# Optimization experiments

Measured on AMD Instinct MI355X. Metric: run time of the kernel, lower is better.

The kernel has to match this reference:

```python
import jax, jax.numpy as jnp
import numpy as np

B, C, H, W = 8, 64, 112, 112
O, K, PAD, STRIDE = 64, 3, 1, 1
KK = K * K
OH = (H - K + 2 * PAD) // STRIDE + 1
OW = (W - K + 2 * PAD) // STRIDE + 1
L = OH * OW  # number of patches


def setup_inputs() -> dict:
    key = jax.random.key(0)
    k1, k2, k3 = jax.random.split(key, 3)
    x = jax.random.normal(k1, (B, C, H, W), dtype=jnp.float32)
    weight = jax.random.normal(k2, (O, C, K, K), dtype=jnp.float32)
    # one uniformly random kernel position to zero out, per patch (nums=1)
    mask_idx = jax.random.randint(k3, (L,), 0, KK, dtype=jnp.int32)
    return {"x": x, "weight": weight, "mask_idx": mask_idx}


def reference(x, weight, mask_idx):
    b = x.shape[0]
    # im2col: [b, C*KK, OH, OW], feature dim ordered channel-major (c, kh, kw)
    # which matches torch.nn.Unfold ordering.
    patches = jax.lax.conv_general_dilated_patches(
        x, (K, K), (STRIDE, STRIDE), ((PAD, PAD), (PAD, PAD)))
    patches = patches.reshape(b, C * KK, L)  # [b, CK, L]

    # Per-patch mask over kernel positions, tiled across channels
    # (equivalent to mask.repeat(1, in_channels) in the original).
    mask = jnp.ones((L, KK), dtype=x.dtype).at[jnp.arange(L), mask_idx].set(0.0)
    mask_full = jnp.tile(mask, (1, C))  # [L, C*KK]

    # weight.view(O, -1).t() -> [CK, O]; masking the weight rows per patch is
    # mathematically identical to masking the unfolded input per patch, which
    # avoids materializing the [L, CK, O] masked weight tensor.
    w2 = weight.reshape(O, C * KK).T  # [CK, O]
    out = jnp.einsum('bkl,lk,ko->bol', patches, mask_full, w2)  # [b, O, L]
    return out.reshape(b, O, OH, OW)
```

## Files before the change

kernel.cpp:

```cpp
#include <hip/hip_runtime.h>
#include <hip/hip_bf16.h>
#include <cstdint>

#define Bn 8
#define Cn 64
#define Hn 112
#define Wn 112
#define On 64
#define Ln (Hn * Wn)
#define HP 114
#define WP 114

typedef __attribute__((ext_vector_type(4)))  float f32x4;
typedef __attribute__((ext_vector_type(16))) float f32x16;
typedef __attribute__((ext_vector_type(8)))  short bf16x8;
typedef __attribute__((ext_vector_type(4)))  unsigned int u32x4;

__device__ __forceinline__ unsigned f2bf(float f) {
    unsigned u = __float_as_uint(f);
    unsigned r = 0x7fffu + ((u >> 16) & 1u);
    return (u + r) >> 16;
}

__global__ __launch_bounds__(64) void wpack_kernel(const float* __restrict__ w,
                                                   unsigned short* __restrict__ wpk) {
    int idx = blockIdx.x;
    int kc = idx & 3, wr = (idx >> 2) & 1, p = idx >> 3;
    int lane = threadIdx.x;
    int o  = wr * 32 + (lane & 31);
    int cb = kc * 16 + (lane >> 5) * 8;
    unsigned pk[4];
#pragma unroll
    for (int j = 0; j < 4; j++) {
        float v0 = w[((size_t)o * Cn + cb + 2 * j) * 9 + p];
        float v1 = w[((size_t)o * Cn + cb + 2 * j + 1) * 9 + p];
        pk[j] = f2bf(v0) | (f2bf(v1) << 16);
    }
    u32x4 v; v[0] = pk[0]; v[1] = pk[1]; v[2] = pk[2]; v[3] = pk[3];
    reinterpret_cast<u32x4*>(wpk)[idx * 64 + lane] = v;
}

__global__ __launch_bounds__(512, 4) void conv_fused(const float* __restrict__ x,
                                                     const unsigned short* __restrict__ wpk,
                                                     const int* __restrict__ mask_idx,
                                                     float* __restrict__ out) {
    __shared__ char xs[4 * WP * Cn * 2];

    int b  = blockIdx.x & 7;
    int lt = blockIdx.x >> 3;
    int l0 = lt * 128;
    int oh0 = l0 / Wn;

    int tid  = threadIdx.x;
    int wave = tid >> 6, lane = tid & 63;
    int wr = wave >> 2;
    int wc = wave & 3;
    int hi = lane >> 5;

    int lg = l0 + wc * 32 + (lane & 31);
    int oh = lg / Wn, ow = lg - oh * Wn;
    int r  = oh - oh0;
    int mv = mask_idx[lg];

    const u32x4* wv = reinterpret_cast<const u32x4*>(wpk);
    u32x4 apre[2][4];
#pragma unroll
    for (int kc = 0; kc < 4; ++kc) apre[0][kc] = wv[((0 * 2 + wr) * 4 + kc) * 64 + lane];
#pragma unroll
    for (int kc = 0; kc < 4; ++kc) apre[1][kc] = wv[((1 * 2 + wr) * 4 + kc) * 64 + lane];

    const float* xb = x + (size_t)b * Cn * Hn * Wn;
#pragma unroll
    for (int it = 0; it < 8; ++it) {
        int q = tid + it * 512;
        if (q < 4 * 8 * WP) {
            int row = q / (8 * WP);
            int rem = q - row * (8 * WP);
            int c8  = rem / WP;
            int wp  = rem - c8 * WP;
            int h = oh0 + row - 1;
            int w = wp - 1;
            bool inb = ((unsigned)h < (unsigned)Hn) & ((unsigned)w < (unsigned)Wn);
            const float* s = xb + ((size_t)(c8 * 8) * Hn + (inb ? h : 0)) * Wn + (inb ? w : 0);
            unsigned pk[4];
#pragma unroll
            for (int j = 0; j < 4; ++j) {
                float v0 = s[(size_t)(2 * j)     * (Hn * Wn)];
                float v1 = s[(size_t)(2 * j + 1) * (Hn * Wn)];
                if (!inb) { v0 = 0.f; v1 = 0.f; }
                pk[j] = f2bf(v0) | (f2bf(v1) << 16);
            }
            int qs = (row * WP + wp) * 8 + c8;
            int off = (qs * 16) ^ ((wp & 7) << 4);
            u32x4 v; v[0] = pk[0]; v[1] = pk[1]; v[2] = pk[2]; v[3] = pk[3];
            *reinterpret_cast<u32x4*>(xs + off) = v;
        }
    }

    f32x16 acc = {};
    const u32x4 vzero = {0u, 0u, 0u, 0u};

    __syncthreads();

#pragma unroll
    for (int p = 0; p < 9; ++p) {
        int dh = p / 3, dw = p - dh * 3;

        int wq   = ow + dw;
        int base = ((r + dh) * WP + wq) << 7;
        int swz  = (wq & 7) << 4;
        u32x4 bv[4];
#pragma unroll
        for (int kc = 0; kc < 4; ++kc) {
            int off = (base + ((2 * kc + hi) << 4)) ^ swz;
            bv[kc] = *reinterpret_cast<const u32x4*>(xs + off);
        }
        if (mv == p) { bv[0] = vzero; bv[1] = vzero; bv[2] = vzero; bv[3] = vzero; }

#pragma unroll
        for (int kc = 0; kc < 4; ++kc) {
            bf16x8 a = *reinterpret_cast<bf16x8*>(&apre[p & 1][kc]);
            bf16x8 bb = *reinterpret_cast<bf16x8*>(&bv[kc]);
            acc = __builtin_amdgcn_mfma_f32_32x32x16_bf16(a, bb, acc, 0, 0, 0);
        }

        if (p < 7) {
#pragma unroll
            for (int kc = 0; kc < 4; ++kc)
                apre[p & 1][kc] = wv[(((p + 2) * 2 + wr) * 4 + kc) * 64 + lane];
        }
    }

    float* ob = out + (size_t)(b * On + wr * 32) * Ln + lg;
#pragma unroll
    for (int reg = 0; reg < 16; ++reg) {
        int orow = (reg & 3) + 8 * (reg >> 2) + 4 * hi;
        ob[(size_t)orow * Ln] = acc[reg];
    }
}

extern "C" void kernel_launch(void* const* d_in, const int* in_sizes, int n_in,
                              void* d_out, int out_size, void* d_ws, size_t ws_size,
                              hipStream_t stream) {
    const float* x    = (const float*)d_in[0];
    const float* w    = (const float*)d_in[1];
    const int*   mask = (const int*)d_in[2];
    float* out = (float*)d_out;

    unsigned short* wpk = (unsigned short*)d_ws;

    wpack_kernel<<<72,      64,  0, stream>>>(w, wpk);
    conv_fused  <<<Bn * 98, 512, 0, stream>>>(x, wpk, mask, out);
}
```

Before: 95.28 us.

## Pre-pack padded bf16 input in prep kernel and stream tiles via global_load_lds

A separate prep pass now converts x into a zero-padded, channel-swizzled bf16 NHWC buffer in workspace, merged into one launch with the weight packing. The conv kernel then fills its LDS tile with direct global_load_lds copies instead of strided fp32 gathers and per-element conversion. This removes redundant halo-row conversion and strided reads from the main kernel. In exchange it adds a full write and re-read of a roughly 13 MB intermediate buffer and an extra pass over x.

```diff
diff --git a/kernel.cpp b/kernel.cpp
--- a/kernel.cpp
+++ b/kernel.cpp
@@ -16,34 +16,70 @@
 typedef __attribute__((ext_vector_type(8)))  short bf16x8;
 typedef __attribute__((ext_vector_type(4)))  unsigned int u32x4;
 
+typedef __attribute__((address_space(3))) unsigned int lds_u32;
+typedef __attribute__((address_space(1))) const unsigned int glob_u32;
+
 __device__ __forceinline__ unsigned f2bf(float f) {
     unsigned u = __float_as_uint(f);
     unsigned r = 0x7fffu + ((u >> 16) & 1u);
     return (u + r) >> 16;
 }
 
-__global__ __launch_bounds__(64) void wpack_kernel(const float* __restrict__ w,
+__global__ __launch_bounds__(128) void prep_kernel(const float* __restrict__ x,
+                                                   const float* __restrict__ w,
+                                                   unsigned short* __restrict__ xps,
                                                    unsigned short* __restrict__ wpk) {
-    int idx = blockIdx.x;
-    int kc = idx & 3, wr = (idx >> 2) & 1, p = idx >> 3;
-    int lane = threadIdx.x;
-    int o  = wr * 32 + (lane & 31);
-    int cb = kc * 16 + (lane >> 5) * 8;
-    unsigned pk[4];
+    int blk = blockIdx.x;
+    int t = threadIdx.x;
+    if (blk < 912) {
+        int b = blk / HP, row = blk - b * HP;
+        int c8  = t >> 4;
+        int wpl = t & 15;
+        int h = row - 1;
+        const float* xb = x + (size_t)b * Cn * Hn * Wn;
+        unsigned short* dst = xps + ((size_t)(b * HP + row) * WP) * Cn;
 #pragma unroll
-    for (int j = 0; j < 4; j++) {
-        float v0 = w[((size_t)o * Cn + cb + 2 * j) * 9 + p];
-        float v1 = w[((size_t)o * Cn + cb + 2 * j + 1) * 9 + p];
-        pk[j] = f2bf(v0) | (f2bf(v1) << 16);
+        for (int g = 0; g < 8; ++g) {
+            int wp = wpl + (g << 4);
+            if (wp < WP) {
+                int wcol = wp - 1;
+                bool inb = ((unsigned)h < (unsigned)Hn) & ((unsigned)wcol < (unsigned)Wn);
+                const float* s = xb + ((size_t)(c8 * 8) * Hn + (inb ? h : 0)) * Wn + (inb ? wcol : 0);
+                unsigned pk[4];
+#pragma unroll
+                for (int j = 0; j < 4; ++j) {
+                    float v0 = s[(size_t)(2 * j)     * (Hn * Wn)];
+                    float v1 = s[(size_t)(2 * j + 1) * (Hn * Wn)];
+                    if (!inb) { v0 = 0.f; v1 = 0.f; }
+                    pk[j] = f2bf(v0) | (f2bf(v1) << 16);
+                }
+                int slot = c8 ^ (wp & 7);
+                u32x4 v; v[0] = pk[0]; v[1] = pk[1]; v[2] = pk[2]; v[3] = pk[3];
+                *reinterpret_cast<u32x4*>(dst + ((size_t)wp * 8 + slot) * 8) = v;
+            }
+        }
+    } else {
+        int idx = (blk - 912) * 2 + (t >> 6);
+        int lane = t & 63;
+        int kc = idx & 3, wr2 = (idx >> 2) & 1, p = idx >> 3;
+        int o  = wr2 * 32 + (lane & 31);
+        int cb = kc * 16 + (lane >> 5) * 8;
+        unsigned pk[4];
+#pragma unroll
+        for (int j = 0; j < 4; ++j) {
+            float v0 = w[((size_t)o * Cn + cb + 2 * j) * 9 + p];
+            float v1 = w[((size_t)o * Cn + cb + 2 * j + 1) * 9 + p];
+            pk[j] = f2bf(v0) | (f2bf(v1) << 16);
+        }
+        u32x4 v; v[0] = pk[0]; v[1] = pk[1]; v[2] = pk[2]; v[3] = pk[3];
+        reinterpret_cast<u32x4*>(wpk)[idx * 64 + lane] = v;
     }
-    u32x4 v; v[0] = pk[0]; v[1] = pk[1]; v[2] = pk[2]; v[3] = pk[3];
-    reinterpret_cast<u32x4*>(wpk)[idx * 64 + lane] = v;
 }
 
-__global__ __launch_bounds__(512, 4) void conv_fused(const float* __restrict__ x,
-                                                     const unsigned short* __restrict__ wpk,
-                                                     const int* __restrict__ mask_idx,
-                                                     float* __restrict__ out) {
+__global__ __launch_bounds__(512, 4) void conv_mfma(const unsigned short* __restrict__ xps,
+                                                    const unsigned short* __restrict__ wpk,
+                                                    const int* __restrict__ mask_idx,
+                                                    float* __restrict__ out) {
     __shared__ char xs[4 * WP * Cn * 2];
 
     int b  = blockIdx.x & 7;
@@ -62,40 +98,27 @@
     int r  = oh - oh0;
     int mv = mask_idx[lg];
 
+    {
+        const char* gsrc = (const char*)(xps + ((size_t)(b * HP + oh0) * WP) * Cn);
+        int cb0 = wave * 456;
+#pragma unroll
+        for (int i = 0; i < 8; ++i) {
+            int cbase = cb0 + i * 64;
+            if (i < 7 || lane < 8) {
+                __builtin_amdgcn_global_load_lds(
+                    (glob_u32*)(gsrc + ((size_t)(cbase + lane) << 4)),
+                    reinterpret_cast<lds_u32*>(reinterpret_cast<uintptr_t>(xs + ((size_t)cbase << 4))),
+                    16, 0, 0);
+            }
+        }
+    }
+
     const u32x4* wv = reinterpret_cast<const u32x4*>(wpk);
     u32x4 apre[2][4];
 #pragma unroll
-    for (int kc = 0; kc < 4; ++kc) apre[0][kc] = wv[((0 * 2 + wr) * 4 + kc) * 64 + lane];
+    for (int kc = 0; kc < 4; ++kc) apre[0][kc] = wv[(wr * 4 + kc) * 64 + lane];
 #pragma unroll
-    for (int kc = 0; kc < 4; ++kc) apre[1][kc] = wv[((1 * 2 + wr) * 4 + kc) * 64 + lane];
-
-    const float* xb = x + (size_t)b * Cn * Hn * Wn;
-#pragma unroll
-    for (int it = 0; it < 8; ++it) {
-        int q = tid + it * 512;
-        if (q < 4 * 8 * WP) {
-            int row = q / (8 * WP);
-            int rem = q - row * (8 * WP);
-            int c8  = rem / WP;
-            int wp  = rem - c8 * WP;
-            int h = oh0 + row - 1;
-            int w = wp - 1;
-            bool inb = ((unsigned)h < (unsigned)Hn) & ((unsigned)w < (unsigned)Wn);
-            const float* s = xb + ((size_t)(c8 * 8) * Hn + (inb ? h : 0)) * Wn + (inb ? w : 0);
-            unsigned pk[4];
-#pragma unroll
-            for (int j = 0; j < 4; ++j) {
-                float v0 = s[(size_t)(2 * j)     * (Hn * Wn)];
-                float v1 = s[(size_t)(2 * j + 1) * (Hn * Wn)];
-                if (!inb) { v0 = 0.f; v1 = 0.f; }
-                pk[j] = f2bf(v0) | (f2bf(v1) << 16);
-            }
-            int qs = (row * WP + wp) * 8 + c8;
-            int off = (qs * 16) ^ ((wp & 7) << 4);
-            u32x4 v; v[0] = pk[0]; v[1] = pk[1]; v[2] = pk[2]; v[3] = pk[3];
-            *reinterpret_cast<u32x4*>(xs + off) = v;
-        }
-    }
+    for (int kc = 0; kc < 4; ++kc) apre[1][kc] = wv[((2 + wr) * 4 + kc) * 64 + lane];
 
     f32x16 acc = {};
     const u32x4 vzero = {0u, 0u, 0u, 0u};
@@ -119,7 +142,7 @@
 
 #pragma unroll
         for (int kc = 0; kc < 4; ++kc) {
-            bf16x8 a = *reinterpret_cast<bf16x8*>(&apre[p & 1][kc]);
+            bf16x8 a  = *reinterpret_cast<bf16x8*>(&apre[p & 1][kc]);
             bf16x8 bb = *reinterpret_cast<bf16x8*>(&bv[kc]);
             acc = __builtin_amdgcn_mfma_f32_32x32x16_bf16(a, bb, acc, 0, 0, 0);
         }
@@ -147,8 +170,9 @@
     const int*   mask = (const int*)d_in[2];
     float* out = (float*)d_out;
 
-    unsigned short* wpk = (unsigned short*)d_ws;
+    unsigned short* xps = (unsigned short*)d_ws;
+    unsigned short* wpk = (unsigned short*)((char*)d_ws + 13307904);
 
-    wpack_kernel<<<72,      64,  0, stream>>>(w, wpk);
-    conv_fused  <<<Bn * 98, 512, 0, stream>>>(x, wpk, mask, out);
+    prep_kernel<<<948,     128, 0, stream>>>(x, w, xps, wpk);
+    conv_mfma  <<<Bn * 98, 512, 0, stream>>>(xps, wpk, mask, out);
 }
```

Measured after the change: 97.73 us. +2.6%, slower.

## Halve block to 256 threads, each wave computing all 64 output channels

Applied to the files above, without the earlier changes.

Each block now has four waves instead of eight, and each wave covers 32 patches for both 32-channel output halves, using two accumulators. Every B fragment read from LDS therefore feeds two MFMAs, which halves LDS reads per MFMA. Weight fragments for one kernel position are prefetched a step ahead into double-buffered registers. The cost is more registers per thread and fewer threads to stage the shared tile, so each thread does more global-load iterations.

```diff
diff --git a/kernel.cpp b/kernel.cpp
--- a/kernel.cpp
+++ b/kernel.cpp
@@ -40,7 +40,7 @@
     reinterpret_cast<u32x4*>(wpk)[idx * 64 + lane] = v;
 }
 
-__global__ __launch_bounds__(512, 4) void conv_fused(const float* __restrict__ x,
+__global__ __launch_bounds__(256, 2) void conv_fused(const float* __restrict__ x,
                                                      const unsigned short* __restrict__ wpk,
                                                      const int* __restrict__ mask_idx,
                                                      float* __restrict__ out) {
@@ -53,26 +53,18 @@
 
     int tid  = threadIdx.x;
     int wave = tid >> 6, lane = tid & 63;
-    int wr = wave >> 2;
-    int wc = wave & 3;
     int hi = lane >> 5;
+    int li = lane & 31;
 
-    int lg = l0 + wc * 32 + (lane & 31);
+    int lg = l0 + wave * 32 + li;
     int oh = lg / Wn, ow = lg - oh * Wn;
     int r  = oh - oh0;
     int mv = mask_idx[lg];
 
-    const u32x4* wv = reinterpret_cast<const u32x4*>(wpk);
-    u32x4 apre[2][4];
-#pragma unroll
-    for (int kc = 0; kc < 4; ++kc) apre[0][kc] = wv[((0 * 2 + wr) * 4 + kc) * 64 + lane];
-#pragma unroll
-    for (int kc = 0; kc < 4; ++kc) apre[1][kc] = wv[((1 * 2 + wr) * 4 + kc) * 64 + lane];
-
     const float* xb = x + (size_t)b * Cn * Hn * Wn;
 #pragma unroll
-    for (int it = 0; it < 8; ++it) {
-        int q = tid + it * 512;
+    for (int it = 0; it < 15; ++it) {
+        int q = tid + it * 256;
         if (q < 4 * 8 * WP) {
             int row = q / (8 * WP);
             int rem = q - row * (8 * WP);
@@ -97,15 +89,27 @@
         }
     }
 
-    f32x16 acc = {};
+    const u32x4* wv = reinterpret_cast<const u32x4*>(wpk);
+    u32x4 af0[8], af1[8];
+#pragma unroll
+    for (int f = 0; f < 8; ++f) af0[f] = wv[f * 64 + lane];
+
+    f32x16 acc0 = {}, acc1 = {};
     const u32x4 vzero = {0u, 0u, 0u, 0u};
 
     __syncthreads();
 
 #pragma unroll
     for (int p = 0; p < 9; ++p) {
+        u32x4* cur = (p & 1) ? af1 : af0;
+        u32x4* nxt = (p & 1) ? af0 : af1;
+        if (p < 8) {
+#pragma unroll
+            for (int f = 0; f < 8; ++f)
+                nxt[f] = wv[((p + 1) * 8 + f) * 64 + lane];
+        }
+
         int dh = p / 3, dw = p - dh * 3;
-
         int wq   = ow + dw;
         int base = ((r + dh) * WP + wq) << 7;
         int swz  = (wq & 7) << 4;
@@ -119,23 +123,20 @@
 
 #pragma unroll
         for (int kc = 0; kc < 4; ++kc) {
-            bf16x8 a = *reinterpret_cast<bf16x8*>(&apre[p & 1][kc]);
             bf16x8 bb = *reinterpret_cast<bf16x8*>(&bv[kc]);
-            acc = __builtin_amdgcn_mfma_f32_32x32x16_bf16(a, bb, acc, 0, 0, 0);
-        }
-
-        if (p < 7) {
-#pragma unroll
-            for (int kc = 0; kc < 4; ++kc)
-                apre[p & 1][kc] = wv[(((p + 2) * 2 + wr) * 4 + kc) * 64 + lane];
+            bf16x8 a0 = *reinterpret_cast<bf16x8*>(&cur[kc]);
+            bf16x8 a1 = *reinterpret_cast<bf16x8*>(&cur[4 + kc]);
+            acc0 = __builtin_amdgcn_mfma_f32_32x32x16_bf16(a0, bb, acc0, 0, 0, 0);
+            acc1 = __builtin_amdgcn_mfma_f32_32x32x16_bf16(a1, bb, acc1, 0, 0, 0);
         }
     }
 
-    float* ob = out + (size_t)(b * On + wr * 32) * Ln + lg;
+    float* ob = out + (size_t)(b * On) * Ln + lg;
 #pragma unroll
     for (int reg = 0; reg < 16; ++reg) {
         int orow = (reg & 3) + 8 * (reg >> 2) + 4 * hi;
-        ob[(size_t)orow * Ln] = acc[reg];
+        ob[(size_t)orow * Ln]        = acc0[reg];
+        ob[(size_t)(orow + 32) * Ln] = acc1[reg];
     }
 }
 
@@ -150,5 +151,5 @@
     unsigned short* wpk = (unsigned short*)d_ws;
 
     wpack_kernel<<<72,      64,  0, stream>>>(w, wpk);
-    conv_fused  <<<Bn * 98, 512, 0, stream>>>(x, wpk, mask, out);
+    conv_fused  <<<Bn * 98, 256, 0, stream>>>(x, wpk, mask, out);
 }
```

Measured after the change: 98.06 us. +2.9%, slower.
